# Performance work log

Measured on AMD Instinct MI355X. Metric: run time of the kernel, lower is better.

## Reference

```python
import jax, jax.numpy as jnp
import numpy as np

BST_DEPTH = 6
NB_SPLIT = 2**BST_DEPTH - 1          # 63 internal (split) nodes
NB_NODES = 2**(BST_DEPTH + 1) - 1    # 127 total nodes (heap layout)
SPLIT = np.arange(NB_SPLIT)
DESC_L = 2 * SPLIT + 1               # left children of split nodes
DESC_R = 2 * SPLIT + 2               # right children of split nodes


def setup_inputs() -> dict:
    key = jax.random.key(0)
    kx, ka = jax.random.split(key)
    x = jax.random.normal(kx, (131072, 512), dtype=jnp.float32)
    A = jax.random.uniform(ka, (NB_SPLIT, 512), dtype=jnp.float32)  # torch.rand init
    return {"x": x, "A": A}


def _compute_q(x, A):
    # XA[:, t] is the split score of internal node t; XA == XA[:, split_nodes]
    XA = x @ A.T                                         # [N, nb_split]
    q = jnp.ones((x.shape[0], NB_NODES), dtype=XA.dtype)  # [N, nb_nodes]
    # Seed children of each split node. NOTE: sequential semantics matter —
    # the right-child write reads q[:, SPLIT] AFTER the left-child write
    # (odd-indexed split nodes were just updated), matching torch in-place ops.
    q = q.at[:, DESC_L].set(jnp.minimum(q[:, SPLIT], XA))
    q = q.at[:, DESC_R].set(jnp.minimum(q[:, SPLIT], -XA))
    # Propagate the running min from parents down the tree, one sweep per level.
    for _ in range(BST_DEPTH):
        q = q.at[:, DESC_L].set(jnp.minimum(q[:, DESC_L], q[:, SPLIT]))
        q = q.at[:, DESC_R].set(jnp.minimum(q[:, DESC_R], q[:, SPLIT]))
    return q


def reference(x, A):
    q = _compute_q(x, A)
    z = jnp.clip(q, 0.0, 1.0)  # pruned=False: no QP pruning branch
    return z
```

## Files before the change

kernel.cpp:

```cpp
#include <hip/hip_runtime.h>
#include <hip/hip_bf16.h>
#include <cstdint>

#define KD 512
#define BM 128
#define NT 512
#define NSPLIT 63
#define NNODES 127
#define BH_OFF 32768
#define BL_OFF 40960

typedef __attribute__((ext_vector_type(8))) short bf16x8;
typedef __attribute__((ext_vector_type(4))) float f32x4;

#define MFMA_B16(a, b, c) __builtin_amdgcn_mfma_f32_16x16x32_bf16(a, b, c, 0, 0, 0)
#define SCHED_FENCE() __builtin_amdgcn_sched_barrier(0)

static __device__ __forceinline__ unsigned short f2bf(float f) {
    return __builtin_bit_cast(unsigned short, __float2bfloat16(f));
}
static __device__ __forceinline__ float bf2f(unsigned short h) {
    return __builtin_bit_cast(float, (unsigned)h << 16);
}
static __device__ __forceinline__ unsigned pack2(float f0, float f1) {
    return (unsigned)f2bf(f0) | ((unsigned)f2bf(f1) << 16);
}

static __device__ __forceinline__ void cvt8(f32x4 a, f32x4 b, bf16x8& hi, bf16x8& lo) {
    const unsigned short h0 = f2bf(a[0]), h1 = f2bf(a[1]), h2 = f2bf(a[2]), h3 = f2bf(a[3]);
    const unsigned short h4 = f2bf(b[0]), h5 = f2bf(b[1]), h6 = f2bf(b[2]), h7 = f2bf(b[3]);
    uint4 H = make_uint4((unsigned)h0 | ((unsigned)h1 << 16), (unsigned)h2 | ((unsigned)h3 << 16),
                         (unsigned)h4 | ((unsigned)h5 << 16), (unsigned)h6 | ((unsigned)h7 << 16));
    uint4 L = make_uint4(pack2(a[0] - bf2f(h0), a[1] - bf2f(h1)),
                         pack2(a[2] - bf2f(h2), a[3] - bf2f(h3)),
                         pack2(b[0] - bf2f(h4), b[1] - bf2f(h5)),
                         pack2(b[2] - bf2f(h6), b[3] - bf2f(h7)));
    hi = __builtin_bit_cast(bf16x8, H);
    lo = __builtin_bit_cast(bf16x8, L);
}

static __device__ __forceinline__ void gload_lds16(const void* g, void* l) {
    __builtin_amdgcn_global_load_lds(
        (const __attribute__((address_space(1))) unsigned int*)g,
        (__attribute__((address_space(3))) unsigned int*)l, 16, 0, 0);
}

template<int N> static __device__ __forceinline__ void vmwait() {
    if constexpr (N == 4)      asm volatile("s_waitcnt vmcnt(4)" ::: "memory");
    else if constexpr (N == 2) asm volatile("s_waitcnt vmcnt(2)" ::: "memory");
    else                       asm volatile("s_waitcnt vmcnt(0)" ::: "memory");
}

template<int T>
static __device__ __forceinline__ void tree_walk16(float qt, const float* __restrict__ srow,
                                                   float* __restrict__ zrow, int part16) {
    const float s  = srow[T];
    const float ql = fminf(qt, s);
    const float qr = fminf(qt, -s);
    if (((2 * T + 1) >> 3) == part16) zrow[2 * T + 1] = fminf(fmaxf(ql, 0.f), 1.f);
    if (((2 * T + 2) >> 3) == part16) zrow[2 * T + 2] = fminf(fmaxf(qr, 0.f), 1.f);
    if constexpr (2 * T + 1 < NSPLIT) tree_walk16<2 * T + 1>(ql, srow, zrow, part16);
    if constexpr (2 * T + 2 < NSPLIT) tree_walk16<2 * T + 2>(qr, srow, zrow, part16);
}

static __device__ __forceinline__ void write_B(unsigned char* lds, int brow, int sl,
                                               bool bvalid, f32x4 b0, f32x4 b1) {
    if (!bvalid) { b0 = (f32x4)(0.f); b1 = (f32x4)(0.f); }
    bf16x8 hi, lo;
    cvt8(b0, b1, hi, lo);
    *reinterpret_cast<bf16x8*>(lds + BH_OFF + brow * 128 + sl * 16) = hi;
    *reinterpret_cast<bf16x8*>(lds + BL_OFF + brow * 128 + sl * 16) = lo;
}

template<int T>
static __device__ __forceinline__ void tiles(
        const float* xsrc, unsigned char* xw, unsigned char* lds,
        const float* ag, bool bvalid, int brow, int sl,
        int va_off, int fr, int g, f32x4 (&acc)[4], f32x4& bn0, f32x4& bn1) {
    if constexpr ((T & 1) == 0 && T > 0) {
        SCHED_FENCE();
        __builtin_amdgcn_s_barrier();
        write_B(lds, brow, sl, bvalid, bn0, bn1);
        asm volatile("s_waitcnt lgkmcnt(0)" ::: "memory");
        __builtin_amdgcn_s_barrier();
        SCHED_FENCE();
        if constexpr (T / 2 + 1 < 8) {
            if (bvalid) {
                bn0 = *reinterpret_cast<const f32x4*>(ag + (T / 2 + 1) * 64);
                bn1 = *reinterpret_cast<const f32x4*>(ag + (T / 2 + 1) * 64 + 4);
            }
        }
        SCHED_FENCE();
    }
    if constexpr (T + 1 < 16) {
        unsigned char* nb = xw + ((T + 1) & 1) * 2048;
        gload_lds16(xsrc + (T + 1) * 32, nb);
        gload_lds16(xsrc + (T + 1) * 32 + 8 * KD, nb + 1024);
    }
    SCHED_FENCE();
    vmwait<((T & 1) == 0 && T <= 12) ? 4 : ((T == 15) ? 0 : 2)>();
    SCHED_FENCE();

    const unsigned char* xbf = xw + (T & 1) * 2048;
    f32x4 va = *reinterpret_cast<const f32x4*>(xbf + va_off);
    f32x4 vb = *reinterpret_cast<const f32x4*>(xbf + (va_off ^ 16));
    bf16x8 ah, al;
    cvt8(va, vb, ah, al);

    const int m   = fr & 7;
    const int bof = fr * 128 + ((((T & 1) * 4) + g) ^ m) * 16;
    const unsigned char* bh = lds + BH_OFF + bof;
    bf16x8 b0 = *reinterpret_cast<const bf16x8*>(bh);
    bf16x8 b1 = *reinterpret_cast<const bf16x8*>(bh + 2048);
    bf16x8 b2 = *reinterpret_cast<const bf16x8*>(bh + 4096);
    bf16x8 b3 = *reinterpret_cast<const bf16x8*>(bh + 6144);
    acc[0] = MFMA_B16(ah, b0, acc[0]);
    acc[1] = MFMA_B16(ah, b1, acc[1]);
    acc[2] = MFMA_B16(ah, b2, acc[2]);
    acc[3] = MFMA_B16(ah, b3, acc[3]);
    acc[0] = MFMA_B16(al, b0, acc[0]);
    acc[1] = MFMA_B16(al, b1, acc[1]);
    acc[2] = MFMA_B16(al, b2, acc[2]);
    acc[3] = MFMA_B16(al, b3, acc[3]);
    const unsigned char* blp = lds + BL_OFF + bof;
    b0 = *reinterpret_cast<const bf16x8*>(blp);
    b1 = *reinterpret_cast<const bf16x8*>(blp + 2048);
    b2 = *reinterpret_cast<const bf16x8*>(blp + 4096);
    b3 = *reinterpret_cast<const bf16x8*>(blp + 6144);
    acc[0] = MFMA_B16(ah, b0, acc[0]);
    acc[1] = MFMA_B16(ah, b1, acc[1]);
    acc[2] = MFMA_B16(ah, b2, acc[2]);
    acc[3] = MFMA_B16(ah, b3, acc[3]);

    if constexpr (T + 1 < 16)
        tiles<T + 1>(xsrc, xw, lds, ag, bvalid, brow, sl, va_off, fr, g, acc, bn0, bn1);
}

__global__ __launch_bounds__(NT, 6)
void lt_mfma11(const float* __restrict__ x, const float* __restrict__ A,
               float* __restrict__ out) {
    __shared__ __align__(16) unsigned char lds[49152];

    const int tid  = threadIdx.x;
    const int wave = tid >> 6;
    const int lane = tid & 63;
    const int fr   = lane & 15;
    const int g    = lane >> 4;
    const int r0   = blockIdx.x * BM;

    unsigned char* xw = lds + wave * 4096;
    const float* xsrc = x + (size_t)(r0 + wave * 16 + (lane >> 3)) * KD
                          + (((lane & 7) ^ ((lane >> 3) & 7)) << 2);
    const int brow = tid >> 3;
    const int bq   = tid & 7;
    const int sl   = bq ^ (brow & 7);
    const bool bvalid = brow < NSPLIT;
    const float* ag = A + (size_t)brow * KD + bq * 8;
    const int va_off = (fr << 7) + (((2 * g) ^ (fr & 7)) << 4);

    f32x4 acc[4];
#pragma unroll
    for (int j = 0; j < 4; ++j) acc[j] = (f32x4)(0.f);

    f32x4 bn0 = (f32x4)(0.f), bn1 = (f32x4)(0.f);
    if (bvalid) {
        bn0 = *reinterpret_cast<const f32x4*>(ag);
        bn1 = *reinterpret_cast<const f32x4*>(ag + 4);
    }
    gload_lds16(xsrc, xw);
    gload_lds16(xsrc + 8 * KD, xw + 1024);
    SCHED_FENCE();
    write_B(lds, brow, sl, bvalid, bn0, bn1);
    asm volatile("s_waitcnt lgkmcnt(0)" ::: "memory");
    __builtin_amdgcn_s_barrier();
    if (bvalid) {
        bn0 = *reinterpret_cast<const f32x4*>(ag + 64);
        bn1 = *reinterpret_cast<const f32x4*>(ag + 68);
    }
    SCHED_FENCE();

    tiles<0>(xsrc, xw, lds, ag, bvalid, brow, sl, va_off, fr, g, acc, bn0, bn1);

    float* warea = reinterpret_cast<float*>(xw);
    float* zw    = warea + 260;
    const int o      = lane >> 4;
    const int part16 = lane & 15;

#pragma unroll
    for (int s = 0; s < 4; ++s) {
        if (g == s) {
#pragma unroll
            for (int nf = 0; nf < 4; ++nf)
#pragma unroll
                for (int rg = 0; rg < 4; ++rg)
                    warea[rg * 65 + nf * 16 + fr] = acc[nf][rg];
        }
        const float* srow = warea + o * 65;
        float* zrow = zw + o * NNODES;
        if (part16 == 0) zrow[0] = 1.f;
        tree_walk16<0>(1.f, srow, zrow, part16);

        float* og = out + (size_t)(r0 + wave * 16 + s * 4) * NNODES;
#pragma unroll
        for (int j = 0; j < 2; ++j) {
            const int idx = j * 64 + lane;
            if (idx < 127)
                *reinterpret_cast<f32x4*>(og + idx * 4) =
                    *reinterpret_cast<const f32x4*>(zw + idx * 4);
        }
    }
}

extern "C" void kernel_launch(void* const* d_in, const int* in_sizes, int n_in,
                              void* d_out, int out_size, void* d_ws, size_t ws_size,
                              hipStream_t stream) {
    const float* x = (const float*)d_in[0];
    const float* A = (const float*)d_in[1];
    float* out = (float*)d_out;
    const int nrows = in_sizes[0] / KD;
    const int grid = nrows / BM;
    lt_mfma11<<<dim3(grid), dim3(NT), 0, stream>>>(x, A, out);
}
```

Measured before the change: 94.81 us.

## Precompute split bf16 A in a prep kernel and triple-buffer B tiles

```diff
diff --git a/kernel.cpp b/kernel.cpp
--- a/kernel.cpp
+++ b/kernel.cpp
@@ -7,8 +7,6 @@
 #define NT 512
 #define NSPLIT 63
 #define NNODES 127
-#define BH_OFF 32768
-#define BL_OFF 40960
 
 typedef __attribute__((ext_vector_type(8))) short bf16x8;
 typedef __attribute__((ext_vector_type(4))) float f32x4;
@@ -46,7 +44,7 @@
 }
 
 template<int N> static __device__ __forceinline__ void vmwait() {
-    if constexpr (N == 4)      asm volatile("s_waitcnt vmcnt(4)" ::: "memory");
+    if constexpr (N == 3)      asm volatile("s_waitcnt vmcnt(3)" ::: "memory");
     else if constexpr (N == 2) asm volatile("s_waitcnt vmcnt(2)" ::: "memory");
     else                       asm volatile("s_waitcnt vmcnt(0)" ::: "memory");
 }
@@ -63,57 +61,50 @@
     if constexpr (2 * T + 2 < NSPLIT) tree_walk16<2 * T + 2>(qr, srow, zrow, part16);
 }
 
-static __device__ __forceinline__ void write_B(unsigned char* lds, int brow, int sl,
-                                               bool bvalid, f32x4 b0, f32x4 b1) {
-    if (!bvalid) { b0 = (f32x4)(0.f); b1 = (f32x4)(0.f); }
+__global__ __launch_bounds__(256)
+void lt_prep(const float* __restrict__ A, unsigned short* __restrict__ ws) {
+    const int gid = blockIdx.x * 256 + threadIdx.x;
+    const int r   = gid >> 6;
+    const int sk  = gid & 63;
+    const int k   = sk << 3;
+    f32x4 a = (f32x4)(0.f), b = (f32x4)(0.f);
+    if (r < NSPLIT) {
+        a = *reinterpret_cast<const f32x4*>(A + (size_t)r * KD + k);
+        b = *reinterpret_cast<const f32x4*>(A + (size_t)r * KD + k + 4);
+    }
     bf16x8 hi, lo;
-    cvt8(b0, b1, hi, lo);
-    *reinterpret_cast<bf16x8*>(lds + BH_OFF + brow * 128 + sl * 16) = hi;
-    *reinterpret_cast<bf16x8*>(lds + BL_OFF + brow * 128 + sl * 16) = lo;
+    cvt8(a, b, hi, lo);
+    const int chunk = sk >> 2;
+    const int sl    = (sk & 3) ^ (r & 3);
+    unsigned short* p = ws + chunk * 4096 + r * 32 + sl * 8;
+    *reinterpret_cast<bf16x8*>(p)        = hi;
+    *reinterpret_cast<bf16x8*>(p + 2048) = lo;
 }
 
 template<int T>
 static __device__ __forceinline__ void tiles(
-        const float* xsrc, unsigned char* xw, unsigned char* lds,
-        const float* ag, bool bvalid, int brow, int sl,
-        int va_off, int fr, int g, f32x4 (&acc)[4], f32x4& bn0, f32x4& bn1) {
-    if constexpr ((T & 1) == 0 && T > 0) {
-        SCHED_FENCE();
-        __builtin_amdgcn_s_barrier();
-        write_B(lds, brow, sl, bvalid, bn0, bn1);
-        asm volatile("s_waitcnt lgkmcnt(0)" ::: "memory");
-        __builtin_amdgcn_s_barrier();
-        SCHED_FENCE();
-        if constexpr (T / 2 + 1 < 8) {
-            if (bvalid) {
-                bn0 = *reinterpret_cast<const f32x4*>(ag + (T / 2 + 1) * 64);
-                bn1 = *reinterpret_cast<const f32x4*>(ag + (T / 2 + 1) * 64 + 4);
-            }
-        }
-        SCHED_FENCE();
-    }
-    if constexpr (T + 1 < 16) {
-        unsigned char* nb = xw + ((T + 1) & 1) * 2048;
-        gload_lds16(xsrc + (T + 1) * 32, nb);
-        gload_lds16(xsrc + (T + 1) * 32 + 8 * KD, nb + 1024);
-    }
-    SCHED_FENCE();
-    vmwait<((T & 1) == 0 && T <= 12) ? 4 : ((T == 15) ? 0 : 2)>();
-    SCHED_FENCE();
-
-    const unsigned char* xbf = xw + (T & 1) * 2048;
-    f32x4 va = *reinterpret_cast<const f32x4*>(xbf + va_off);
-    f32x4 vb = *reinterpret_cast<const f32x4*>(xbf + (va_off ^ 16));
+        const float* xsl, const unsigned short* bsl, unsigned char* lds, int woff,
+        int bo, f32x4& v0a, f32x4& v0b, f32x4& v1a, f32x4& v1b,
+        f32x4& v2a, f32x4& v2b, f32x4 (&acc)[4]) {
+    if constexpr (T + 2 < 16) {
+        gload_lds16(bsl + (T + 2) * 4096, lds + ((T + 2) % 3) * 8192 + woff);
+        constexpr int S = (T + 2) % 3;
+        f32x4& na = (S == 0) ? v0a : (S == 1) ? v1a : v2a;
+        f32x4& nb = (S == 0) ? v0b : (S == 1) ? v1b : v2b;
+        na = *reinterpret_cast<const f32x4*>(xsl + (T + 2) * 32);
+        nb = *reinterpret_cast<const f32x4*>(xsl + (T + 2) * 32 + 4);
+    }
+    constexpr int C = T % 3;
+    const f32x4& ca = (C == 0) ? v0a : (C == 1) ? v1a : v2a;
+    const f32x4& cb = (C == 0) ? v0b : (C == 1) ? v1b : v2b;
     bf16x8 ah, al;
-    cvt8(va, vb, ah, al);
-
-    const int m   = fr & 7;
-    const int bof = fr * 128 + ((((T & 1) * 4) + g) ^ m) * 16;
-    const unsigned char* bh = lds + BH_OFF + bof;
-    bf16x8 b0 = *reinterpret_cast<const bf16x8*>(bh);
-    bf16x8 b1 = *reinterpret_cast<const bf16x8*>(bh + 2048);
-    bf16x8 b2 = *reinterpret_cast<const bf16x8*>(bh + 4096);
-    bf16x8 b3 = *reinterpret_cast<const bf16x8*>(bh + 6144);
+    cvt8(ca, cb, ah, al);
+
+    const unsigned char* bb = lds + C * 8192;
+    bf16x8 b0 = *reinterpret_cast<const bf16x8*>(bb + bo);
+    bf16x8 b1 = *reinterpret_cast<const bf16x8*>(bb + bo + 1024);
+    bf16x8 b2 = *reinterpret_cast<const bf16x8*>(bb + bo + 2048);
+    bf16x8 b3 = *reinterpret_cast<const bf16x8*>(bb + bo + 3072);
     acc[0] = MFMA_B16(ah, b0, acc[0]);
     acc[1] = MFMA_B16(ah, b1, acc[1]);
     acc[2] = MFMA_B16(ah, b2, acc[2]);
@@ -122,24 +113,30 @@
     acc[1] = MFMA_B16(al, b1, acc[1]);
     acc[2] = MFMA_B16(al, b2, acc[2]);
     acc[3] = MFMA_B16(al, b3, acc[3]);
-    const unsigned char* blp = lds + BL_OFF + bof;
-    b0 = *reinterpret_cast<const bf16x8*>(blp);
-    b1 = *reinterpret_cast<const bf16x8*>(blp + 2048);
-    b2 = *reinterpret_cast<const bf16x8*>(blp + 4096);
-    b3 = *reinterpret_cast<const bf16x8*>(blp + 6144);
+    b0 = *reinterpret_cast<const bf16x8*>(bb + 4096 + bo);
+    b1 = *reinterpret_cast<const bf16x8*>(bb + 4096 + bo + 1024);
+    b2 = *reinterpret_cast<const bf16x8*>(bb + 4096 + bo + 2048);
+    b3 = *reinterpret_cast<const bf16x8*>(bb + 4096 + bo + 3072);
     acc[0] = MFMA_B16(ah, b0, acc[0]);
     acc[1] = MFMA_B16(ah, b1, acc[1]);
     acc[2] = MFMA_B16(ah, b2, acc[2]);
     acc[3] = MFMA_B16(ah, b3, acc[3]);
 
-    if constexpr (T + 1 < 16)
-        tiles<T + 1>(xsrc, xw, lds, ag, bvalid, brow, sl, va_off, fr, g, acc, bn0, bn1);
+    if constexpr (T < 15) {
+        SCHED_FENCE();
+        vmwait<(T <= 13) ? 3 : 0>();
+        SCHED_FENCE();
+        __builtin_amdgcn_s_barrier();
+        SCHED_FENCE();
+        tiles<T + 1>(xsl, bsl, lds, woff, bo,
+                     v0a, v0b, v1a, v1b, v2a, v2b, acc);
+    }
 }
 
 __global__ __launch_bounds__(NT, 6)
-void lt_mfma11(const float* __restrict__ x, const float* __restrict__ A,
+void lt_mfma12(const float* __restrict__ x, const unsigned short* __restrict__ ws,
                float* __restrict__ out) {
-    __shared__ __align__(16) unsigned char lds[49152];
+    __shared__ __align__(16) unsigned char lds[24576];
 
     const int tid  = threadIdx.x;
     const int wave = tid >> 6;
@@ -148,40 +145,33 @@
     const int g    = lane >> 4;
     const int r0   = blockIdx.x * BM;
 
-    unsigned char* xw = lds + wave * 4096;
-    const float* xsrc = x + (size_t)(r0 + wave * 16 + (lane >> 3)) * KD
-                          + (((lane & 7) ^ ((lane >> 3) & 7)) << 2);
-    const int brow = tid >> 3;
-    const int bq   = tid & 7;
-    const int sl   = bq ^ (brow & 7);
-    const bool bvalid = brow < NSPLIT;
-    const float* ag = A + (size_t)brow * KD + bq * 8;
-    const int va_off = (fr << 7) + (((2 * g) ^ (fr & 7)) << 4);
+    const float* xsl = x + (size_t)(r0 + wave * 16 + fr) * KD + g * 8;
+    const unsigned short* bsl = ws + wave * 512 + lane * 8;
+    const int woff = wave * 1024;
+    const int bo = fr * 64 + ((g ^ (fr & 3)) << 4);
 
     f32x4 acc[4];
 #pragma unroll
     for (int j = 0; j < 4; ++j) acc[j] = (f32x4)(0.f);
-
-    f32x4 bn0 = (f32x4)(0.f), bn1 = (f32x4)(0.f);
-    if (bvalid) {
-        bn0 = *reinterpret_cast<const f32x4*>(ag);
-        bn1 = *reinterpret_cast<const f32x4*>(ag + 4);
-    }
-    gload_lds16(xsrc, xw);
-    gload_lds16(xsrc + 8 * KD, xw + 1024);
+    f32x4 v0a = (f32x4)(0.f), v0b = v0a, v1a = v0a, v1b = v0a, v2a = v0a, v2b = v0a;
+
+    gload_lds16(bsl, lds + woff);
+    gload_lds16(bsl + 4096, lds + 8192 + woff);
+    v0a = *reinterpret_cast<const f32x4*>(xsl);
+    v0b = *reinterpret_cast<const f32x4*>(xsl + 4);
+    v1a = *reinterpret_cast<const f32x4*>(xsl + 32);
+    v1b = *reinterpret_cast<const f32x4*>(xsl + 36);
     SCHED_FENCE();
-    write_B(lds, brow, sl, bvalid, bn0, bn1);
-    asm volatile("s_waitcnt lgkmcnt(0)" ::: "memory");
+    vmwait<2>();
+    SCHED_FENCE();
     __builtin_amdgcn_s_barrier();
-    if (bvalid) {
-        bn0 = *reinterpret_cast<const f32x4*>(ag + 64);
-        bn1 = *reinterpret_cast<const f32x4*>(ag + 68);
-    }
     SCHED_FENCE();
 
-    tiles<0>(xsrc, xw, lds, ag, bvalid, brow, sl, va_off, fr, g, acc, bn0, bn1);
-
-    float* warea = reinterpret_cast<float*>(xw);
+    tiles<0>(xsl, bsl, lds, woff, bo, v0a, v0b, v1a, v1b, v2a, v2b, acc);
+
+    __syncthreads();
+
+    float* warea = reinterpret_cast<float*>(lds + wave * 3072);
     float* zw    = warea + 260;
     const int o      = lane >> 4;
     const int part16 = lane & 15;
@@ -217,7 +207,8 @@
     const float* x = (const float*)d_in[0];
     const float* A = (const float*)d_in[1];
     float* out = (float*)d_out;
+    unsigned short* ws = (unsigned short*)d_ws;
     const int nrows = in_sizes[0] / KD;
-    const int grid = nrows / BM;
-    lt_mfma11<<<dim3(grid), dim3(NT), 0, stream>>>(x, A, out);
-}
+    lt_prep<<<dim3(16), dim3(256), 0, stream>>>(A, ws);
+    lt_mfma12<<<dim3(nrows / BM), dim3(NT), 0, stream>>>(x, ws, out);
+}
```

After: 92.06 us. -2.9%, faster.

## Stage x in 128-column chunks with larger LDS and fewer, wider epilogue passes

Applied to the files above, without the earlier changes.

```diff
diff --git a/kernel.cpp b/kernel.cpp
--- a/kernel.cpp
+++ b/kernel.cpp
@@ -7,8 +7,8 @@
 #define NT 512
 #define NSPLIT 63
 #define NNODES 127
-#define BH_OFF 32768
-#define BL_OFF 40960
+#define BH_OFF 65536
+#define BL_OFF 73728
 
 typedef __attribute__((ext_vector_type(8))) short bf16x8;
 typedef __attribute__((ext_vector_type(4))) float f32x4;
@@ -46,21 +46,20 @@
 }
 
 template<int N> static __device__ __forceinline__ void vmwait() {
-    if constexpr (N == 4)      asm volatile("s_waitcnt vmcnt(4)" ::: "memory");
-    else if constexpr (N == 2) asm volatile("s_waitcnt vmcnt(2)" ::: "memory");
-    else                       asm volatile("s_waitcnt vmcnt(0)" ::: "memory");
+    if constexpr (N == 2) asm volatile("s_waitcnt vmcnt(2)" ::: "memory");
+    else                  asm volatile("s_waitcnt vmcnt(0)" ::: "memory");
 }
 
 template<int T>
-static __device__ __forceinline__ void tree_walk16(float qt, const float* __restrict__ srow,
-                                                   float* __restrict__ zrow, int part16) {
+static __device__ __forceinline__ void tree_walk8(float qt, const float* __restrict__ srow,
+                                                  float* __restrict__ zrow, int p8) {
     const float s  = srow[T];
     const float ql = fminf(qt, s);
     const float qr = fminf(qt, -s);
-    if (((2 * T + 1) >> 3) == part16) zrow[2 * T + 1] = fminf(fmaxf(ql, 0.f), 1.f);
-    if (((2 * T + 2) >> 3) == part16) zrow[2 * T + 2] = fminf(fmaxf(qr, 0.f), 1.f);
-    if constexpr (2 * T + 1 < NSPLIT) tree_walk16<2 * T + 1>(ql, srow, zrow, part16);
-    if constexpr (2 * T + 2 < NSPLIT) tree_walk16<2 * T + 2>(qr, srow, zrow, part16);
+    if (((2 * T + 1) >> 4) == p8) zrow[2 * T + 1] = fminf(fmaxf(ql, 0.f), 1.f);
+    if (((2 * T + 2) >> 4) == p8) zrow[2 * T + 2] = fminf(fmaxf(qr, 0.f), 1.f);
+    if constexpr (2 * T + 1 < NSPLIT) tree_walk8<2 * T + 1>(ql, srow, zrow, p8);
+    if constexpr (2 * T + 2 < NSPLIT) tree_walk8<2 * T + 2>(qr, srow, zrow, p8);
 }
 
 static __device__ __forceinline__ void write_B(unsigned char* lds, int brow, int sl,
@@ -72,42 +71,29 @@
     *reinterpret_cast<bf16x8*>(lds + BL_OFF + brow * 128 + sl * 16) = lo;
 }
 
+static __device__ __forceinline__ void stage_x(const float* __restrict__ x, int rbase,
+                                               int rl, int s, int c, unsigned char* xw) {
+#pragma unroll
+    for (int i = 0; i < 8; ++i) {
+        const int row = 2 * i + rl;
+        const float* src = x + (size_t)(rbase + row) * KD + c * 128
+                             + ((s ^ (row & 7)) << 2);
+        gload_lds16(src, xw + i * 1024);
+    }
+}
+
 template<int T>
 static __device__ __forceinline__ void tiles(
-        const float* xsrc, unsigned char* xw, unsigned char* lds,
-        const float* ag, bool bvalid, int brow, int sl,
-        int va_off, int fr, int g, f32x4 (&acc)[4], f32x4& bn0, f32x4& bn1) {
-    if constexpr ((T & 1) == 0 && T > 0) {
-        SCHED_FENCE();
-        __builtin_amdgcn_s_barrier();
-        write_B(lds, brow, sl, bvalid, bn0, bn1);
-        asm volatile("s_waitcnt lgkmcnt(0)" ::: "memory");
-        __builtin_amdgcn_s_barrier();
-        SCHED_FENCE();
-        if constexpr (T / 2 + 1 < 8) {
-            if (bvalid) {
-                bn0 = *reinterpret_cast<const f32x4*>(ag + (T / 2 + 1) * 64);
-                bn1 = *reinterpret_cast<const f32x4*>(ag + (T / 2 + 1) * 64 + 4);
-            }
-        }
-        SCHED_FENCE();
-    }
-    if constexpr (T + 1 < 16) {
-        unsigned char* nb = xw + ((T + 1) & 1) * 2048;
-        gload_lds16(xsrc + (T + 1) * 32, nb);
-        gload_lds16(xsrc + (T + 1) * 32 + 8 * KD, nb + 1024);
-    }
-    SCHED_FENCE();
-    vmwait<((T & 1) == 0 && T <= 12) ? 4 : ((T == 15) ? 0 : 2)>();
-    SCHED_FENCE();
-
-    const unsigned char* xbf = xw + (T & 1) * 2048;
-    f32x4 va = *reinterpret_cast<const f32x4*>(xbf + va_off);
-    f32x4 vb = *reinterpret_cast<const f32x4*>(xbf + (va_off ^ 16));
+        const float* __restrict__ x, int rbase, int rl, int s, unsigned char* xw,
+        unsigned char* lds, const float* ag, bool bvalid, int brow, int sl,
+        int fr, int g, f32x4 (&acc)[4], f32x4& bn0, f32x4& bn1) {
+    const int m  = fr & 7;
+    const int uv = (T & 3) * 8 + g * 2;
+    f32x4 va = *reinterpret_cast<const f32x4*>(xw + fr * 512 + ((uv ^ m) << 4));
+    f32x4 vb = *reinterpret_cast<const f32x4*>(xw + fr * 512 + (((uv + 1) ^ m) << 4));
     bf16x8 ah, al;
     cvt8(va, vb, ah, al);
 
-    const int m   = fr & 7;
     const int bof = fr * 128 + ((((T & 1) * 4) + g) ^ m) * 16;
     const unsigned char* bh = lds + BH_OFF + bof;
     bf16x8 b0 = *reinterpret_cast<const bf16x8*>(bh);
@@ -122,24 +108,49 @@
     acc[1] = MFMA_B16(al, b1, acc[1]);
     acc[2] = MFMA_B16(al, b2, acc[2]);
     acc[3] = MFMA_B16(al, b3, acc[3]);
-    const unsigned char* blp = lds + BL_OFF + bof;
-    b0 = *reinterpret_cast<const bf16x8*>(blp);
-    b1 = *reinterpret_cast<const bf16x8*>(blp + 2048);
-    b2 = *reinterpret_cast<const bf16x8*>(blp + 4096);
-    b3 = *reinterpret_cast<const bf16x8*>(blp + 6144);
+    const unsigned char* bl = lds + BL_OFF + bof;
+    b0 = *reinterpret_cast<const bf16x8*>(bl);
+    b1 = *reinterpret_cast<const bf16x8*>(bl + 2048);
+    b2 = *reinterpret_cast<const bf16x8*>(bl + 4096);
+    b3 = *reinterpret_cast<const bf16x8*>(bl + 6144);
     acc[0] = MFMA_B16(ah, b0, acc[0]);
     acc[1] = MFMA_B16(ah, b1, acc[1]);
     acc[2] = MFMA_B16(ah, b2, acc[2]);
     acc[3] = MFMA_B16(ah, b3, acc[3]);
 
+    if constexpr ((T & 1) == 1 && T < 15) {
+        SCHED_FENCE();
+        if constexpr ((T & 3) == 3) {
+            asm volatile("s_waitcnt lgkmcnt(0)" ::: "memory");
+            stage_x(x, rbase, rl, s, (T + 1) / 4, xw);
+        }
+        SCHED_FENCE();
+        __builtin_amdgcn_s_barrier();
+        write_B(lds, brow, sl, bvalid, bn0, bn1);
+        asm volatile("s_waitcnt lgkmcnt(0)" ::: "memory");
+        __builtin_amdgcn_s_barrier();
+        SCHED_FENCE();
+        if constexpr ((T + 3) / 2 <= 7) {
+            if (bvalid) {
+                bn0 = *reinterpret_cast<const f32x4*>(ag + ((T + 3) / 2) * 64);
+                bn1 = *reinterpret_cast<const f32x4*>(ag + ((T + 3) / 2) * 64 + 4);
+            }
+        }
+        SCHED_FENCE();
+        if constexpr ((T & 3) == 3) {
+            vmwait<2>();
+            SCHED_FENCE();
+        }
+    }
     if constexpr (T + 1 < 16)
-        tiles<T + 1>(xsrc, xw, lds, ag, bvalid, brow, sl, va_off, fr, g, acc, bn0, bn1);
-}
-
-__global__ __launch_bounds__(NT, 6)
-void lt_mfma11(const float* __restrict__ x, const float* __restrict__ A,
+        tiles<T + 1>(x, rbase, rl, s, xw, lds, ag, bvalid, brow, sl,
+                     fr, g, acc, bn0, bn1);
+}
+
+__global__ __launch_bounds__(NT, 4)
+void lt_mfma14(const float* __restrict__ x, const float* __restrict__ A,
                float* __restrict__ out) {
-    __shared__ __align__(16) unsigned char lds[49152];
+    __shared__ __align__(16) unsigned char lds[81920];
 
     const int tid  = threadIdx.x;
     const int wave = tid >> 6;
@@ -147,16 +158,17 @@
     const int fr   = lane & 15;
     const int g    = lane >> 4;
     const int r0   = blockIdx.x * BM;
-
-    unsigned char* xw = lds + wave * 4096;
-    const float* xsrc = x + (size_t)(r0 + wave * 16 + (lane >> 3)) * KD
-                          + (((lane & 7) ^ ((lane >> 3) & 7)) << 2);
+    const int rbase = r0 + wave * 16;
+
+    unsigned char* xw = lds + wave * 8192;
+    const int rl = lane >> 5;
+    const int s  = lane & 31;
+
     const int brow = tid >> 3;
     const int bq   = tid & 7;
     const int sl   = bq ^ (brow & 7);
     const bool bvalid = brow < NSPLIT;
     const float* ag = A + (size_t)brow * KD + bq * 8;
-    const int va_off = (fr << 7) + (((2 * g) ^ (fr & 7)) << 4);
 
     f32x4 acc[4];
 #pragma unroll
@@ -167,8 +179,7 @@
         bn0 = *reinterpret_cast<const f32x4*>(ag);
         bn1 = *reinterpret_cast<const f32x4*>(ag + 4);
     }
-    gload_lds16(xsrc, xw);
-    gload_lds16(xsrc + 8 * KD, xw + 1024);
+    stage_x(x, rbase, rl, s, 0, xw);
     SCHED_FENCE();
     write_B(lds, brow, sl, bvalid, bn0, bn1);
     asm volatile("s_waitcnt lgkmcnt(0)" ::: "memory");
@@ -178,33 +189,35 @@
         bn1 = *reinterpret_cast<const f32x4*>(ag + 68);
     }
     SCHED_FENCE();
-
-    tiles<0>(xsrc, xw, lds, ag, bvalid, brow, sl, va_off, fr, g, acc, bn0, bn1);
+    vmwait<2>();
+    SCHED_FENCE();
+
+    tiles<0>(x, rbase, rl, s, xw, lds, ag, bvalid, brow, sl, fr, g, acc, bn0, bn1);
 
     float* warea = reinterpret_cast<float*>(xw);
-    float* zw    = warea + 260;
-    const int o      = lane >> 4;
-    const int part16 = lane & 15;
-
-#pragma unroll
-    for (int s = 0; s < 4; ++s) {
-        if (g == s) {
+    float* zw    = warea + 520;
+    const int o  = lane >> 3;
+    const int p8 = lane & 7;
+
+#pragma unroll
+    for (int sp = 0; sp < 2; ++sp) {
+        if ((g >> 1) == sp) {
 #pragma unroll
             for (int nf = 0; nf < 4; ++nf)
 #pragma unroll
                 for (int rg = 0; rg < 4; ++rg)
-                    warea[rg * 65 + nf * 16 + fr] = acc[nf][rg];
+                    warea[((g & 1) * 4 + rg) * 65 + nf * 16 + fr] = acc[nf][rg];
         }
         const float* srow = warea + o * 65;
         float* zrow = zw + o * NNODES;
-        if (part16 == 0) zrow[0] = 1.f;
-        tree_walk16<0>(1.f, srow, zrow, part16);
-
-        float* og = out + (size_t)(r0 + wave * 16 + s * 4) * NNODES;
-#pragma unroll
-        for (int j = 0; j < 2; ++j) {
+        if (p8 == 0) zrow[0] = 1.f;
+        tree_walk8<0>(1.f, srow, zrow, p8);
+
+        float* og = out + (size_t)(rbase + sp * 8) * NNODES;
+#pragma unroll
+        for (int j = 0; j < 4; ++j) {
             const int idx = j * 64 + lane;
-            if (idx < 127)
+            if (idx < 254)
                 *reinterpret_cast<f32x4*>(og + idx * 4) =
                     *reinterpret_cast<const f32x4*>(zw + idx * 4);
         }
@@ -219,5 +232,5 @@
     float* out = (float*)d_out;
     const int nrows = in_sizes[0] / KD;
     const int grid = nrows / BM;
-    lt_mfma11<<<dim3(grid), dim3(NT), 0, stream>>>(x, A, out);
-}
+    lt_mfma14<<<dim3(grid), dim3(NT), 0, stream>>>(x, A, out);
+}
```

After: 84.34 us. 11.0% less time.
